# Kernel tuning notes

Hardware: AMD Instinct MI355X
Metric: run time of the kernel (lower is better)

## Reference

```python
import jax, jax.numpy as jnp
import numpy as np

COMMA_ID = 1010  # ',' in bert-base-uncased vocab
N_HEADS = 8
BN_EPS = 1e-5


def setup_inputs() -> dict:
    key = jax.random.key(0)
    ks = jax.random.split(key, 12)
    B, S, D = 64, 512, 768
    sc = 0.02
    text_hs = jax.random.normal(ks[0], (B, S, D), jnp.float32)
    cols_hs = jax.random.normal(ks[1], (B, S, D), jnp.float32)
    # column input ids: random non-comma tokens, commas planted every 16 positions -> 32 commas/row, 33 segments
    col_ids = jax.random.randint(ks[2], (B, S), 2000, 30000, dtype=jnp.int32)
    col_ids = col_ids.at[:, ::16].set(COMMA_ID)
    Wq = jax.random.normal(ks[3], (D, D), jnp.float32) * sc
    Wk = jax.random.normal(ks[4], (D, D), jnp.float32) * sc
    Wv = jax.random.normal(ks[5], (D, D), jnp.float32) * sc
    Wo = jax.random.normal(ks[6], (D, D), jnp.float32) * sc
    bq = jnp.zeros((D,), jnp.float32)
    bk = jnp.zeros((D,), jnp.float32)
    bv = jnp.zeros((D,), jnp.float32)
    bo = jnp.zeros((D,), jnp.float32)
    gamma = jnp.ones((S,), jnp.float32)
    beta = jnp.zeros((S,), jnp.float32)
    w_out = jax.random.normal(ks[7], (D, 1), jnp.float32) * sc
    b_out = jnp.zeros((1,), jnp.float32)
    return {"text_hs": text_hs, "cols_hs": cols_hs, "col_ids": col_ids, "n_segments": 33,
            "Wq": Wq, "bq": bq, "Wk": Wk, "bk": bk, "Wv": Wv, "bv": bv, "Wo": Wo, "bo": bo,
            "gamma": gamma, "beta": beta, "w_out": w_out, "b_out": b_out}


def reference(text_hs, cols_hs, col_ids, n_segments,
              Wq, bq, Wk, bk, Wv, bv, Wo, bo, gamma, beta, w_out, b_out):
    B, S, D = text_hs.shape
    hd = D // N_HEADS
    # cross attention: query = columns, key/value = text (torch MultiheadAttention, batch_first)
    q = (cols_hs @ Wq.T + bq).reshape(B, S, N_HEADS, hd)
    k = (text_hs @ Wk.T + bk).reshape(B, S, N_HEADS, hd)
    v = (text_hs @ Wv.T + bv).reshape(B, S, N_HEADS, hd)
    scores = jnp.einsum('bqhd,bkhd->bhqk', q, k) / jnp.sqrt(jnp.asarray(hd, q.dtype))
    attn = jax.nn.softmax(scores, axis=-1)
    o = jnp.einsum('bhqk,bkhd->bqhd', attn, v).reshape(B, S, D)
    attn_out = o @ Wo.T + bo  # [B,S,D]
    # BatchNorm1d(S) in training mode: per-seq-position channel stats over (batch, D)
    mean = attn_out.mean(axis=(0, 2), keepdims=True)
    var = jnp.mean((attn_out - mean) ** 2, axis=(0, 2), keepdims=True)
    bn = (attn_out - mean) / jnp.sqrt(var + BN_EPS) * gamma[None, :, None] + beta[None, :, None]
    # residual add + scalar head -> per-token score [B,S]
    ret = ((cols_hs + bn) @ w_out + b_out)[..., 0]
    # compose_outputs: segment-sum over comma-delimited spans, comma tokens excluded
    is_comma = col_ids == COMMA_ID
    seg = jnp.cumsum(is_comma.astype(jnp.int32), axis=1)  # commas before each non-comma token
    vals = jnp.where(is_comma, jnp.zeros((), ret.dtype), ret)
    flat_seg = (jnp.arange(B, dtype=jnp.int32)[:, None] * n_segments + seg).reshape(-1)
    out = jax.ops.segment_sum(vals.reshape(-1), flat_seg, num_segments=B * n_segments)
    return out.reshape(B, n_segments)
```

## Files before the change

kernel.cpp:

```cpp
#include <hip/hip_runtime.h>
#include <hip/hip_bf16.h>
#include <math.h>

typedef __attribute__((ext_vector_type(8))) short bf16x8;
typedef __attribute__((ext_vector_type(4))) float f32x4;

#define COMMA_ID 1010
#define S 512
#define D 768
#define NH 8
#define HD 96

__device__ __forceinline__ ushort f2bf(float f) {
  union { float f; unsigned u; } v; v.f = f;
  unsigned u = v.u;
  return (ushort)((u + 0x7fffu + ((u >> 16) & 1u)) >> 16);
}
__device__ __forceinline__ float bf2f(ushort h) {
  union { unsigned u; float f; } v; v.u = ((unsigned)h) << 16; return v.f;
}

__device__ __forceinline__ void async16(void* lds, const void* g) {
  __builtin_amdgcn_global_load_lds(
      (const __attribute__((address_space(1))) unsigned int*)g,
      (__attribute__((address_space(3))) unsigned int*)lds, 16, 0, 0);
}

__device__ __forceinline__ f32x4 mfma16(bf16x8 a, bf16x8 b, f32x4 c) {
  return __builtin_amdgcn_mfma_f32_16x16x32_bf16(a, b, c, 0, 0, 0);
}

__global__ __launch_bounds__(256) void cvt2_kernel(const float* __restrict__ a, ushort* __restrict__ oa,
                                                   const float* __restrict__ b, ushort* __restrict__ ob_,
                                                   int n8each) {
  int i = blockIdx.x * 256 + threadIdx.x;
  const float* in; ushort* out; int j;
  if (i < n8each) { in = a; out = oa; j = i; }
  else { in = b; out = ob_; j = i - n8each; if (j >= n8each) return; }
  const float4* p = ((const float4*)in) + (size_t)j * 2;
  float4 x = p[0], y = p[1];
  bf16x8 o;
  o[0] = (short)f2bf(x.x); o[1] = (short)f2bf(x.y); o[2] = (short)f2bf(x.z); o[3] = (short)f2bf(x.w);
  o[4] = (short)f2bf(y.x); o[5] = (short)f2bf(y.y); o[6] = (short)f2bf(y.z); o[7] = (short)f2bf(y.w);
  ((bf16x8*)out)[j] = o;
}

__global__ __launch_bounds__(256) void cvtW_kernel(
    const float* __restrict__ w0, const float* __restrict__ w1,
    const float* __restrict__ w2, const float* __restrict__ w3,
    ushort* __restrict__ o0, ushort* __restrict__ o1,
    ushort* __restrict__ o2, ushort* __restrict__ o3,
    int n8, float sc0) {
  int i = blockIdx.x * 256 + threadIdx.x;
  int sel = i / n8, j = i - sel * n8;
  if (sel >= 4) return;
  const float* in = sel == 0 ? w0 : sel == 1 ? w1 : sel == 2 ? w2 : w3;
  ushort* out = sel == 0 ? o0 : sel == 1 ? o1 : sel == 2 ? o2 : o3;
  float sc = sel == 0 ? sc0 : 1.0f;
  const float4* p = ((const float4*)in) + (size_t)j * 2;
  float4 x = p[0], y = p[1];
  bf16x8 o;
  o[0] = (short)f2bf(x.x * sc); o[1] = (short)f2bf(x.y * sc); o[2] = (short)f2bf(x.z * sc); o[3] = (short)f2bf(x.w * sc);
  o[4] = (short)f2bf(y.x * sc); o[5] = (short)f2bf(y.y * sc); o[6] = (short)f2bf(y.z * sc); o[7] = (short)f2bf(y.w * sc);
  ((bf16x8*)out)[j] = o;
}

#define BM 128
#define BN 128
#define BK 32

template<int MODE>
__global__ __launch_bounds__(256) void gemm_bf16(
    const ushort* __restrict__ A, const ushort* __restrict__ W,
    const float* __restrict__ bias, float bscale, ushort* __restrict__ Cout,
    const float* __restrict__ wv, float* __restrict__ sum_s,
    float* __restrict__ sq_s, float* __restrict__ c2,
    int M, int N, int K)
{
  const int NT = N / BN;
  int nwg = gridDim.x, cpx = nwg >> 3;
  int l = (blockIdx.x & 7) * cpx + (blockIdx.x >> 3);
  int mt = l / NT, nt = l % NT;
  int m0 = mt * BM, n0 = nt * BN;
  int tid = threadIdx.x;
  int w = tid >> 6, lane = tid & 63;
  int wr = w >> 1, wc = w & 1;
  int lr = lane & 15, ks = lane >> 4;
  __shared__ __align__(16) ushort As[2][BM * BK];
  __shared__ __align__(16) ushort Bs[2][BN * BK];
  f32x4 acc[4][4] = {};
  const ushort* Arow = A + (size_t)m0 * K;
  const ushort* Wrow = W + (size_t)n0 * K;
  int srow = tid >> 2, sch = tid & 3;

  auto STAGE = [&](int buf, int k0) {
#pragma unroll
    for (int i = 0; i < 2; ++i) {
      int idx = i * 256 + tid;
      async16(&As[buf][idx * 8], Arow + (size_t)(i * 64 + srow) * K + k0 + sch * 8);
      async16(&Bs[buf][idx * 8], Wrow + (size_t)(i * 64 + srow) * K + k0 + sch * 8);
    }
  };
  auto COMPUTE = [&](int buf) {
    bf16x8 a[4], b[4];
#pragma unroll
    for (int m = 0; m < 4; m++) a[m] = *(const bf16x8*)&As[buf][(wr * 64 + m * 16 + lr) * BK + ks * 8];
#pragma unroll
    for (int n = 0; n < 4; n++) b[n] = *(const bf16x8*)&Bs[buf][(wc * 64 + n * 16 + lr) * BK + ks * 8];
#pragma unroll
    for (int m = 0; m < 4; m++)
#pragma unroll
      for (int n = 0; n < 4; n++)
        acc[m][n] = mfma16(a[m], b[n], acc[m][n]);
  };

  STAGE(0, 0);
  __syncthreads();
  int cur = 0;
  for (int k0 = BK; k0 < K; k0 += BK) {
    STAGE(cur ^ 1, k0);
    COMPUTE(cur);
    __syncthreads();
    cur ^= 1;
  }
  COMPUTE(cur);

  float bnv[4];
#pragma unroll
  for (int n = 0; n < 4; n++) bnv[n] = bias[n0 + wc * 64 + n * 16 + lr] * bscale;

  if (MODE == 0) {
#pragma unroll
    for (int m = 0; m < 4; m++) {
      int grow = m0 + wr * 64 + m * 16 + ks * 4;
#pragma unroll
      for (int r = 0; r < 4; r++) {
        ushort* cp = Cout + (size_t)(grow + r) * N + n0 + wc * 64 + lr;
#pragma unroll
        for (int n = 0; n < 4; n++) cp[n * 16] = f2bf(acc[m][n][r] + bnv[n]);
      }
    }
  } else {
    float wn[4];
#pragma unroll
    for (int n = 0; n < 4; n++) wn[n] = wv[n0 + wc * 64 + n * 16 + lr];
#pragma unroll
    for (int m = 0; m < 4; m++) {
#pragma unroll
      for (int r = 0; r < 4; r++) {
        float ps = 0.f, pq = 0.f, pw = 0.f;
#pragma unroll
        for (int n = 0; n < 4; n++) {
          float v = acc[m][n][r] + bnv[n];
          ps += v; pq += v * v; pw += v * wn[n];
        }
#pragma unroll
        for (int mk = 1; mk < 16; mk <<= 1) {
          ps += __shfl_xor(ps, mk);
          pq += __shfl_xor(pq, mk);
          pw += __shfl_xor(pw, mk);
        }
        if (lr == 0) {
          int grow = m0 + wr * 64 + m * 16 + ks * 4 + r;
          atomicAdd(&sum_s[grow & (S - 1)], ps);
          atomicAdd(&sq_s[grow & (S - 1)], pq);
          atomicAdd(&c2[grow], pw);
        }
      }
    }
  }
}

__global__ __launch_bounds__(256) void transpose_v(const ushort* __restrict__ vb,
                                                   ushort* __restrict__ vt) {
  int blk = blockIdx.x;
  int dt = blk % 3; int st = (blk / 3) % (S / 32); int h = (blk / (3 * (S / 32))) % NH;
  int b = blk / (3 * (S / 32) * NH);
  __shared__ ushort t[32][33];
  int i = threadIdx.x >> 5, j = threadIdx.x & 31;
  int s0 = st * 32, d0 = dt * 32;
#pragma unroll
  for (int k = 0; k < 4; k++) {
    int s = s0 + i + k * 8;
    t[i + k * 8][j] = vb[((size_t)(b * S + s)) * D + h * HD + d0 + j];
  }
  __syncthreads();
#pragma unroll
  for (int k = 0; k < 4; k++) {
    int d = d0 + i + k * 8;
    vt[((size_t)((b * NH + h) * HD + d)) * S + s0 + j] = t[j][i + k * 8];
  }
}

__global__ __launch_bounds__(256, 3) void attn_kernel(const ushort* __restrict__ qb,
                                                      const ushort* __restrict__ kb,
                                                      const ushort* __restrict__ vt,
                                                      ushort* __restrict__ ob) {
  int wgid = blockIdx.x;
  int xcd = wgid & 7, t1 = wgid >> 3;
  int qt = t1 & 3, phi = t1 >> 2;
  int p = phi * 8 + xcd;
  int b = p >> 3, h = p & 7;
  int tid = threadIdx.x;
  int w = tid >> 6, lane = tid & 63;
  int lr = lane & 15, ks = lane >> 4;
  int q0 = qt * 128 + w * 32;

  __shared__ __align__(16) ushort Ks[6144];
  __shared__ __align__(16) ushort Vs[2][6144];
  __shared__ __align__(16) ushort Pb[4][1152];
  ushort* Pw = &Pb[w][0];

  const size_t bS = (size_t)b * S;
  const ushort* qptr = qb + (bS + q0 + lr) * D + h * HD;
  bf16x8 aq[2][3];
#pragma unroll
  for (int m = 0; m < 2; m++)
#pragma unroll
    for (int x = 0; x < 3; x++)
      aq[m][x] = *(const bf16x8*)(qptr + (size_t)m * 16 * D + x * 32 + ks * 8);

  float l_part[2][4] = {};
  f32x4 oacc[2][6] = {};

  const ushort* kbase = kb + bS * D + h * HD;
  const ushort* vbase = vt + (size_t)((b * NH + h) * HD) * S;

  auto STAGE_K = [&](int kv0) {
#pragma unroll
    for (int i = 0; i < 3; i++) {
      int c = w + 4 * i;
      async16(&Ks[(c * 64 + lane) * 8], kbase + (size_t)(kv0 + lane) * D + c * 8);
    }
  };
  auto STAGE_V = [&](int buf, int kv0) {
#pragma unroll
    for (int i = 0; i < 3; i++) {
      int u = (w + 4 * i) * 64 + lane;
      int cc = u / 96, d = u - cc * 96;
      async16(&Vs[buf][(size_t)u * 8], vbase + (size_t)d * S + kv0 + cc * 8);
    }
  };

  STAGE_K(0);
  STAGE_V(0, 0);
  __syncthreads();

  for (int it = 0; it < 8; ++it) {
    int cur = it & 1;
    f32x4 st[2][4];
#pragma unroll
    for (int t = 0; t < 4; t++) {
      bf16x8 bk[3];
#pragma unroll
      for (int x = 0; x < 3; x++)
        bk[x] = *(const bf16x8*)&Ks[((x * 4 + ks) * 64 + t * 16 + lr) * 8];
#pragma unroll
      for (int m = 0; m < 2; m++) {
        f32x4 s = {};
        s = mfma16(aq[m][0], bk[0], s);
        s = mfma16(aq[m][1], bk[1], s);
        s = mfma16(aq[m][2], bk[2], s);
        st[m][t] = s;
      }
    }
    __syncthreads();
    if (it < 7) { STAGE_K((it + 1) * 64); STAGE_V(cur ^ 1, (it + 1) * 64); }
    bf16x8 pa[2][2];
#pragma unroll
    for (int m = 0; m < 2; m++) {
#pragma unroll
      for (int t = 0; t < 4; t++)
#pragma unroll
        for (int r = 0; r < 4; r++) {
          float e = exp2f(st[m][t][r]);
          l_part[m][r] += e;
          Pw[(ks * 4 + r) * 72 + t * 16 + lr] = f2bf(e);
        }
#pragma unroll
      for (int kk = 0; kk < 2; kk++)
        pa[m][kk] = *(const bf16x8*)&Pw[lr * 72 + kk * 32 + ks * 8];
    }
    const ushort* Vb = &Vs[cur][0];
#pragma unroll
    for (int kk = 0; kk < 2; kk++)
#pragma unroll
      for (int n = 0; n < 6; n++) {
        bf16x8 bv = *(const bf16x8*)&Vb[((kk * 4 + ks) * 96 + n * 16 + lr) * 8];
        oacc[0][n] = mfma16(pa[0][kk], bv, oacc[0][n]);
        oacc[1][n] = mfma16(pa[1][kk], bv, oacc[1][n]);
      }
    __syncthreads();
  }

  float inv[2][4];
#pragma unroll
  for (int m = 0; m < 2; m++)
#pragma unroll
    for (int r = 0; r < 4; r++) {
      float s = l_part[m][r];
#pragma unroll
      for (int mk = 1; mk < 16; mk <<= 1) s += __shfl_xor(s, mk);
      inv[m][r] = 1.0f / s;
    }
  ushort* optr = ob + (bS + q0) * D + h * HD;
#pragma unroll
  for (int m = 0; m < 2; m++)
#pragma unroll
    for (int n = 0; n < 6; n++)
#pragma unroll
      for (int r = 0; r < 4; r++)
        optr[(size_t)(m * 16 + ks * 4 + r) * D + n * 16 + lr] = f2bf(oacc[m][n][r] * inv[m][r]);
}

__global__ __launch_bounds__(256) void c1_dot(const ushort* __restrict__ colsb,
                                              const float* __restrict__ wv,
                                              float* __restrict__ c1) {
  int row = blockIdx.x * 4 + (threadIdx.x >> 6);
  int lane = threadIdx.x & 63;
  const ushort* rp = colsb + (size_t)row * D;
  float s = 0.f;
  bf16x8 a = *(const bf16x8*)(rp + lane * 8);
#pragma unroll
  for (int j = 0; j < 8; j++) s += bf2f((ushort)a[j]) * wv[lane * 8 + j];
  ushort4 b4 = *(const ushort4*)(rp + 512 + lane * 4);
  s += bf2f(b4.x) * wv[512 + lane * 4 + 0];
  s += bf2f(b4.y) * wv[512 + lane * 4 + 1];
  s += bf2f(b4.z) * wv[512 + lane * 4 + 2];
  s += bf2f(b4.w) * wv[512 + lane * 4 + 3];
#pragma unroll
  for (int mk = 1; mk < 64; mk <<= 1) s += __shfl_xor(s, mk);
  if (lane == 0) c1[row] = s;
}

__global__ __launch_bounds__(512) void finalize_kernel(
    const float* __restrict__ sum_s, const float* __restrict__ sq_s,
    const float* __restrict__ c1, const float* __restrict__ c2,
    const float* __restrict__ gamma, const float* __restrict__ beta,
    const float* __restrict__ wv, const float* __restrict__ b_out,
    const int* __restrict__ ids, float* __restrict__ out, int nseg, float invBD)
{
  int b = blockIdx.x, s = threadIdx.x;
  int wid = s >> 6, lane = s & 63;
  __shared__ float wpart[8];
  __shared__ int wtot[8];
  __shared__ float seg_acc[64];
  float wval = wv[s] + (s < (D - S) ? wv[S + s] : 0.f);
  float t = wval;
#pragma unroll
  for (int mk = 1; mk < 64; mk <<= 1) t += __shfl_xor(t, mk);
  if (lane == 0) wpart[wid] = t;
  int row = b * S + s;
  bool comma = (ids[row] == COMMA_ID);
  unsigned long long mask = __ballot(comma);
  if (lane == 0) wtot[wid] = __popcll(mask);
  if (s < 64) seg_acc[s] = 0.f;
  __syncthreads();
  float Sw = 0.f;
#pragma unroll
  for (int i = 0; i < 8; i++) Sw += wpart[i];
  float mean = sum_s[s] * invBD;
  float var = sq_s[s] * invBD - mean * mean;
  float alpha = gamma[s] * rsqrtf(var + 1e-5f);
  float shift = beta[s] - mean * alpha;
  float ret = c1[row] + b_out[0] + alpha * c2[row] + shift * Sw;
  int base = 0;
  for (int i = 0; i < wid; i++) base += wtot[i];
  int seg = base + __popcll(mask & ((1ull << lane) - 1ull)) + (comma ? 1 : 0);
  if (!comma && seg < nseg) atomicAdd(&seg_acc[seg], ret);
  __syncthreads();
  if (s < nseg) out[b * nseg + s] = seg_acc[s];
}

extern "C" void kernel_launch(void* const* d_in, const int* in_sizes, int n_in,
                              void* d_out, int out_size, void* d_ws, size_t ws_size,
                              hipStream_t stream) {
  const float* text = (const float*)d_in[0];
  const float* cols = (const float*)d_in[1];
  const int* ids = (const int*)d_in[2];
  const float* Wq = (const float*)d_in[4];
  const float* bq = (const float*)d_in[5];
  const float* Wk = (const float*)d_in[6];
  const float* bk = (const float*)d_in[7];
  const float* Wv = (const float*)d_in[8];
  const float* bv = (const float*)d_in[9];
  const float* Wo = (const float*)d_in[10];
  const float* bo = (const float*)d_in[11];
  const float* gamma = (const float*)d_in[12];
  const float* beta = (const float*)d_in[13];
  const float* wv = (const float*)d_in[14];
  const float* b_out = (const float*)d_in[15];

  const int B = in_sizes[0] / (S * D);
  const int M = B * S;
  const int nseg = out_size / B;
  const size_t NE = (size_t)B * S * D;
  const size_t big = NE * 2;
  const float qscale = 0.10206207262f * 1.44269504089f;

  char* ws = (char*)d_ws;
  size_t off = 0;
  auto alloc = [&](size_t bytes) { void* p = ws + off; off = (off + bytes + 255) & ~(size_t)255; return p; };
  ushort* ws0 = (ushort*)alloc(big);
  ushort* ws1 = (ushort*)alloc(big);
  ushort* qb  = (ushort*)alloc(big);
  ushort* kb  = (ushort*)alloc(big);
  ushort* Wq_b = (ushort*)alloc((size_t)D * D * 2);
  ushort* Wk_b = (ushort*)alloc((size_t)D * D * 2);
  ushort* Wv_b = (ushort*)alloc((size_t)D * D * 2);
  ushort* Wo_b = (ushort*)alloc((size_t)D * D * 2);
  float* sum_s = (float*)alloc(S * 4);
  float* sq_s  = (float*)alloc(S * 4);
  float* c1    = (float*)alloc((size_t)M * 4);
  float* c2    = (float*)alloc((size_t)M * 4);

  ushort* text_b = ws0; ushort* cols_b = ws1;
  ushort* vb = ws1;
  ushort* vt = ws0;
  ushort* ob = ws1;

  int n8 = (int)(NE / 8);
  cvt2_kernel<<<(2 * n8 + 255) / 256, 256, 0, stream>>>(text, text_b, cols, cols_b, n8);
  int w8 = D * D / 8;
  cvtW_kernel<<<(4 * w8 + 255) / 256, 256, 0, stream>>>(Wq, Wk, Wv, Wo, Wq_b, Wk_b, Wv_b, Wo_b, w8, qscale);

  hipMemsetAsync(sum_s, 0, S * 4, stream);
  hipMemsetAsync(sq_s, 0, S * 4, stream);
  hipMemsetAsync(c2, 0, (size_t)M * 4, stream);

  c1_dot<<<M / 4, 256, 0, stream>>>(cols_b, wv, c1);

  int ggrid = (M / BM) * (D / BN);
  gemm_bf16<0><<<ggrid, 256, 0, stream>>>(cols_b, Wq_b, bq, qscale, qb, nullptr, nullptr, nullptr, nullptr, M, D, D);
  gemm_bf16<0><<<ggrid, 256, 0, stream>>>(text_b, Wk_b, bk, 1.0f, kb, nullptr, nullptr, nullptr, nullptr, M, D, D);
  gemm_bf16<0><<<ggrid, 256, 0, stream>>>(text_b, Wv_b, bv, 1.0f, vb, nullptr, nullptr, nullptr, nullptr, M, D, D);

  transpose_v<<<B * NH * (S / 32) * 3, 256, 0, stream>>>(vb, vt);

  attn_kernel<<<B * NH * 4, 256, 0, stream>>>(qb, kb, vt, ob);

  gemm_bf16<1><<<ggrid, 256, 0, stream>>>(ob, Wo_b, bo, 1.0f, nullptr, wv, sum_s, sq_s, c2, M, D, D);

  finalize_kernel<<<B, 512, 0, stream>>>(sum_s, sq_s, c1, c2, gamma, beta, wv, b_out, ids,
                                         (float*)d_out, nseg, 1.0f / (float)(B * D));
}
```

Baseline: 469.7 us.

## Deepen GEMM pipeline to four LDS stages with vmcnt-based waits and new LDS layout

Converts the bf16 GEMM from double buffering to a 4-buffer ring with three tiles in flight. It waits on partial vmcnt counts plus raw s_barrier, so the loop no longer drains all global loads every iteration. The LDS layout changes to k-chunk-major (chunk*128+row) to cut bank conflicts on fragment reads, and K is hardcoded to 768. It also adds launch_bounds(256,2), and LDS use doubles to 64KB per block, which may limit occupancy.

Result: slower. 570.5 us (+21.4%).

```diff
diff --git a/kernel.cpp b/kernel.cpp
--- a/kernel.cpp
+++ b/kernel.cpp
@@ -68,14 +68,16 @@
 #define BM 128
 #define BN 128
 #define BK 32
+#define KDIM 768
+#define NTILE (KDIM / BK)
 
 template<int MODE>
-__global__ __launch_bounds__(256) void gemm_bf16(
+__global__ __launch_bounds__(256, 2) void gemm_bf16(
     const ushort* __restrict__ A, const ushort* __restrict__ W,
     const float* __restrict__ bias, float bscale, ushort* __restrict__ Cout,
     const float* __restrict__ wv, float* __restrict__ sum_s,
     float* __restrict__ sq_s, float* __restrict__ c2,
-    int M, int N, int K)
+    int M, int N)
 {
   const int NT = N / BN;
   int nwg = gridDim.x, cpx = nwg >> 3;
@@ -86,27 +88,27 @@
   int w = tid >> 6, lane = tid & 63;
   int wr = w >> 1, wc = w & 1;
   int lr = lane & 15, ks = lane >> 4;
-  __shared__ __align__(16) ushort As[2][BM * BK];
-  __shared__ __align__(16) ushort Bs[2][BN * BK];
+  __shared__ __align__(16) ushort As[4][512 * 8];
+  __shared__ __align__(16) ushort Bs[4][512 * 8];
   f32x4 acc[4][4] = {};
-  const ushort* Arow = A + (size_t)m0 * K;
-  const ushort* Wrow = W + (size_t)n0 * K;
-  int srow = tid >> 2, sch = tid & 3;
+  const ushort* Arow = A + (size_t)m0 * KDIM;
+  const ushort* Wrow = W + (size_t)n0 * KDIM;
+  int srow = tid & 127, c0 = tid >> 7;
 
   auto STAGE = [&](int buf, int k0) {
-#pragma unroll
-    for (int i = 0; i < 2; ++i) {
-      int idx = i * 256 + tid;
-      async16(&As[buf][idx * 8], Arow + (size_t)(i * 64 + srow) * K + k0 + sch * 8);
-      async16(&Bs[buf][idx * 8], Wrow + (size_t)(i * 64 + srow) * K + k0 + sch * 8);
-    }
+    async16(&As[buf][tid * 8],         Arow + (size_t)srow * KDIM + k0 + c0 * 8);
+    async16(&As[buf][(256 + tid) * 8], Arow + (size_t)srow * KDIM + k0 + (2 + c0) * 8);
+    async16(&Bs[buf][tid * 8],         Wrow + (size_t)srow * KDIM + k0 + c0 * 8);
+    async16(&Bs[buf][(256 + tid) * 8], Wrow + (size_t)srow * KDIM + k0 + (2 + c0) * 8);
   };
   auto COMPUTE = [&](int buf) {
+    const ushort* Ab = &As[buf][0];
+    const ushort* Bb = &Bs[buf][0];
     bf16x8 a[4], b[4];
 #pragma unroll
-    for (int m = 0; m < 4; m++) a[m] = *(const bf16x8*)&As[buf][(wr * 64 + m * 16 + lr) * BK + ks * 8];
-#pragma unroll
-    for (int n = 0; n < 4; n++) b[n] = *(const bf16x8*)&Bs[buf][(wc * 64 + n * 16 + lr) * BK + ks * 8];
+    for (int m = 0; m < 4; m++) a[m] = *(const bf16x8*)&Ab[(ks * 128 + wr * 64 + m * 16 + lr) * 8];
+#pragma unroll
+    for (int n = 0; n < 4; n++) b[n] = *(const bf16x8*)&Bb[(ks * 128 + wc * 64 + n * 16 + lr) * 8];
 #pragma unroll
     for (int m = 0; m < 4; m++)
 #pragma unroll
@@ -115,15 +117,31 @@
   };
 
   STAGE(0, 0);
-  __syncthreads();
-  int cur = 0;
-  for (int k0 = BK; k0 < K; k0 += BK) {
-    STAGE(cur ^ 1, k0);
-    COMPUTE(cur);
-    __syncthreads();
-    cur ^= 1;
+  STAGE(1, BK);
+  STAGE(2, 2 * BK);
+  asm volatile("s_waitcnt vmcnt(8)" ::: "memory");
+  __builtin_amdgcn_s_barrier();
+  __builtin_amdgcn_sched_barrier(0);
+
+  for (int t = 0; t < NTILE - 3; ++t) {
+    STAGE((t + 3) & 3, (t + 3) * BK);
+    COMPUTE(t & 3);
+    __builtin_amdgcn_sched_barrier(0);
+    asm volatile("s_waitcnt vmcnt(8)" ::: "memory");
+    __builtin_amdgcn_s_barrier();
+    __builtin_amdgcn_sched_barrier(0);
   }
-  COMPUTE(cur);
+  COMPUTE((NTILE - 3) & 3);
+  __builtin_amdgcn_sched_barrier(0);
+  asm volatile("s_waitcnt vmcnt(4)" ::: "memory");
+  __builtin_amdgcn_s_barrier();
+  __builtin_amdgcn_sched_barrier(0);
+  COMPUTE((NTILE - 2) & 3);
+  __builtin_amdgcn_sched_barrier(0);
+  asm volatile("s_waitcnt vmcnt(0)" ::: "memory");
+  __builtin_amdgcn_s_barrier();
+  __builtin_amdgcn_sched_barrier(0);
+  COMPUTE((NTILE - 1) & 3);
 
   float bnv[4];
 #pragma unroll
@@ -431,15 +449,15 @@
   c1_dot<<<M / 4, 256, 0, stream>>>(cols_b, wv, c1);
 
   int ggrid = (M / BM) * (D / BN);
-  gemm_bf16<0><<<ggrid, 256, 0, stream>>>(cols_b, Wq_b, bq, qscale, qb, nullptr, nullptr, nullptr, nullptr, M, D, D);
-  gemm_bf16<0><<<ggrid, 256, 0, stream>>>(text_b, Wk_b, bk, 1.0f, kb, nullptr, nullptr, nullptr, nullptr, M, D, D);
-  gemm_bf16<0><<<ggrid, 256, 0, stream>>>(text_b, Wv_b, bv, 1.0f, vb, nullptr, nullptr, nullptr, nullptr, M, D, D);
+  gemm_bf16<0><<<ggrid, 256, 0, stream>>>(cols_b, Wq_b, bq, qscale, qb, nullptr, nullptr, nullptr, nullptr, M, D);
+  gemm_bf16<0><<<ggrid, 256, 0, stream>>>(text_b, Wk_b, bk, 1.0f, kb, nullptr, nullptr, nullptr, nullptr, M, D);
+  gemm_bf16<0><<<ggrid, 256, 0, stream>>>(text_b, Wv_b, bv, 1.0f, vb, nullptr, nullptr, nullptr, nullptr, M, D);
 
   transpose_v<<<B * NH * (S / 32) * 3, 256, 0, stream>>>(vb, vt);
 
   attn_kernel<<<B * NH * 4, 256, 0, stream>>>(qb, kb, vt, ob);
 
-  gemm_bf16<1><<<ggrid, 256, 0, stream>>>(ob, Wo_b, bo, 1.0f, nullptr, wv, sum_s, sq_s, c2, M, D, D);
+  gemm_bf16<1><<<ggrid, 256, 0, stream>>>(ob, Wo_b, bo, 1.0f, nullptr, wv, sum_s, sq_s, c2, M, D);
 
   finalize_kernel<<<B, 512, 0, stream>>>(sum_s, sq_s, c1, c2, gamma, beta, wv, b_out, ids,
                                          (float*)d_out, nseg, 1.0f / (float)(B * D));
```
